# Kernel tuning notes

Hardware: AMD Instinct MI355X
Metric: run time of the kernel (lower is better)

## Reference

```python
import jax, jax.numpy as jnp
import numpy as np

B, C, H, W = 4, 384, 56, 56
K, S = 5, 7


def setup_inputs() -> dict:
    key = jax.random.key(0)
    k1, k2, k3, k4, k5 = jax.random.split(key, 5)
    x = jax.random.normal(k1, (B, C, H, W), dtype=jnp.float32)
    ctx = jax.random.normal(k2, (B, C, H, W), dtype=jnp.float32)
    # 1x1 conv weights stored as (out_ch, in_ch) matrices
    Wq = jax.random.normal(k3, (C // 2, C), dtype=jnp.float32) * (1.0 / np.sqrt(C))
    Wk = jax.random.normal(k4, (C // 2, C), dtype=jnp.float32) * (1.0 / np.sqrt(C))
    Wwd = jax.random.normal(k5, (K * K, S * S), dtype=jnp.float32) * (1.0 / np.sqrt(S * S))
    return {"x": x, "ctx": ctx, "Wq": Wq, "Wk": Wk, "Wwd": Wwd}


def reference(x, ctx, Wq, Wk, Wwd):
    b, c, h, w = x.shape
    kk = K
    # q: 1x1 conv then flatten spatial -> (B, C/2, HW)
    q = jnp.einsum('dc,bchw->bdhw', Wq, x).reshape(b, c // 2, h * w)
    # adaptive avg pool to S x S (H,W multiples of S -> uniform 8x8 bins)
    ctx_p = ctx.reshape(b, c, S, h // S, S, w // S).mean(axis=(3, 5))  # (B,C,S,S)
    kf = jnp.einsum('dc,bcst->bdst', Wk, ctx_p).reshape(b, c // 2, S * S)
    # attention over region centers: (B, HW, S*S)
    A = jax.nn.softmax(jnp.einsum('bdn,bds->bns', q, kf), axis=-1)
    # dynamic per-pixel kernels via 1x1 conv S*S -> k*k: (B, k*k, H, W)
    dyn = jnp.einsum('js,bns->bjn', Wwd, A).reshape(b, kk * kk, h, w)
    # unfold x (im2col with padding k//2) -> (B, C, k*k, H, W)
    pad = kk // 2
    xp = jnp.pad(x, ((0, 0), (0, 0), (pad, pad), (pad, pad)))
    patches = jnp.stack(
        [xp[:, :, i:i + h, j:j + w] for i in range(kk) for j in range(kk)], axis=2
    )
    # per-pixel weighted reduction over the k*k taps
    out = jnp.einsum('bcjhw,bjhw->bchw', patches, dyn)
    return out
```

## Files before the change

### kernel.cpp

```cpp
#include <hip/hip_runtime.h>

#define BB 4
#define CCH 384
#define HH 56
#define WWD 56
#define HW 3136
#define S2 49
#define S2P 52
#define D2 192
#define K2 25
#define XSP 20

__global__ __launch_bounds__(256) void gtpool_k(const float* __restrict__ Wa,
                                                const float* __restrict__ Wb,
                                                const float* __restrict__ ctx,
                                                float* __restrict__ GT,
                                                float* __restrict__ P) {
    __shared__ float As[D2 * 16];
    __shared__ float Bs[D2 * 16];
    int blk = blockIdx.x;
    int t = threadIdx.x;
    if (blk < 576) {
        int bi = blk % 24, bj = blk / 24;
        int tj = t & 15, ti = t >> 4;
#pragma unroll
        for (int k = 0; k < 3; k++) {
            int idx = t + 256 * k;
            int d = idx >> 2, q = idx & 3;
            *(float4*)&As[idx * 4] = *(const float4*)&Wa[(size_t)d * CCH + bi * 16 + 4 * q];
            *(float4*)&Bs[idx * 4] = *(const float4*)&Wb[(size_t)d * CCH + bj * 16 + 4 * q];
        }
        __syncthreads();
        float acc = 0.f;
#pragma unroll 8
        for (int d = 0; d < D2; d++)
            acc += As[d * 16 + ti] * Bs[d * 16 + tj];
        GT[(size_t)(bi * 16 + ti) * CCH + bj * 16 + tj] = acc;
    } else {
        int bs = blk - 576;
        int b = bs / S2, s = bs - b * S2;
        int sy = s / 7, sx = s % 7;
        {
            const float* p = ctx + ((size_t)(b * CCH + t)) * HW + sy * 8 * WWD + sx * 8;
            float sum = 0.f;
#pragma unroll
            for (int r = 0; r < 8; r++) {
                float4 a  = *(const float4*)(p + r * WWD);
                float4 c4 = *(const float4*)(p + r * WWD + 4);
                sum += a.x + a.y + a.z + a.w + c4.x + c4.y + c4.z + c4.w;
            }
            P[(size_t)bs * CCH + t] = sum * (1.f / 64.f);
        }
        if (t < 128) {
            int c = t + 256;
            const float* p = ctx + ((size_t)(b * CCH + c)) * HW + sy * 8 * WWD + sx * 8;
            float sum = 0.f;
#pragma unroll
            for (int r = 0; r < 8; r++) {
                float4 a  = *(const float4*)(p + r * WWD);
                float4 c4 = *(const float4*)(p + r * WWD + 4);
                sum += a.x + a.y + a.z + a.w + c4.x + c4.y + c4.z + c4.w;
            }
            P[(size_t)bs * CCH + c] = sum * (1.f / 64.f);
        }
    }
}

__global__ __launch_bounds__(256) void mv2_k(const float* __restrict__ GTt,
                                             const float* __restrict__ P,
                                             float* __restrict__ M) {
    int t = threadIdx.x;
    int r = blockIdx.x * 2 + (t >> 7);
    int c = t & 127;
    int bs0 = c, bs1 = c + 128;
    bool has1 = (bs1 < BB * S2);
    const float4* g4 = (const float4*)(GTt + (size_t)r * CCH);
    const float4* p0 = (const float4*)(P + (size_t)bs0 * CCH);
    const float4* p1 = (const float4*)(P + (size_t)(has1 ? bs1 : bs0) * CCH);
    float a0 = 0.f, a1 = 0.f, a2 = 0.f, a3 = 0.f;
#pragma unroll 8
    for (int i = 0; i < CCH / 4; i++) {
        float4 g  = g4[i];
        float4 q0 = p0[i];
        float4 q1 = p1[i];
        a0 += g.x * q0.x + g.y * q0.y;
        a1 += g.z * q0.z + g.w * q0.w;
        a2 += g.x * q1.x + g.y * q1.y;
        a3 += g.z * q1.z + g.w * q1.w;
    }
    int b0 = bs0 / S2, s0 = bs0 - b0 * S2;
    M[((size_t)(b0 * CCH + r)) * S2P + s0] = a0 + a1;
    if (has1) {
        int b1 = bs1 / S2, s1 = bs1 - b1 * S2;
        M[((size_t)(b1 * CCH + r)) * S2P + s1] = a2 + a3;
    }
    if (c >= 68 && c < 80) {
        int rem = c - 68;
        int bb = rem / 3, sp = 49 + rem % 3;
        M[((size_t)(bb * CCH + r)) * S2P + sp] = 0.f;
    }
}

__global__ __launch_bounds__(256) void attn_k(const float* __restrict__ x,
                                              const float* __restrict__ M,
                                              const float* __restrict__ Wwd,
                                              float* __restrict__ dyn) {
    __shared__ __align__(16) float smem[96 * XSP + 96 * S2P];
    __shared__ __align__(16) float sc[16 * S2P];
    __shared__ __align__(16) float wl[K2 * S2P];
    float* xs  = smem;
    float* Ms  = smem + 96 * XSP;
    float* red = smem;

    int b  = blockIdx.x / 196;
    int n0 = (blockIdx.x % 196) * 16;
    int t  = threadIdx.x;
    int pxg = t & 3, sg = (t >> 2) & 3, slice = t >> 4;

    float4 acc4[4][4];
#pragma unroll
    for (int k = 0; k < 4; k++)
#pragma unroll
        for (int j = 0; j < 4; j++) acc4[k][j] = make_float4(0.f, 0.f, 0.f, 0.f);

    const float* xb = x + (size_t)b * CCH * HW + n0;
    const float* Mb = M + (size_t)b * CCH * S2P;

#pragma unroll
    for (int k = 0; k < 5; k++) {
        int i = t + 256 * k;
        int j = i / S2P, ss = i - j * S2P;
        wl[i] = (ss < S2) ? Wwd[j * S2 + ss] : 0.f;
    }
    if (t < 20) {
        int i = t + 1280;
        int j = i / S2P, ss = i - j * S2P;
        wl[i] = (ss < S2) ? Wwd[j * S2 + ss] : 0.f;
    }

    int r0 = t >> 2, cq = t & 3;
    int r1 = (t + 256) >> 2;
    float4 px0, px1, pm0, pm1, pm2, pm3, pm4;

#define ATTN_LOAD(c0)                                                          \
    {                                                                          \
        px0 = *(const float4*)&xb[(size_t)((c0) + r0) * HW + 4 * cq];          \
        if (t < 128)                                                           \
            px1 = *(const float4*)&xb[(size_t)((c0) + r1) * HW + 4 * cq];      \
        const float* srcm = Mb + (size_t)(c0) * S2P;                           \
        pm0 = *(const float4*)&srcm[4 * t];                                    \
        pm1 = *(const float4*)&srcm[4 * (t + 256)];                            \
        pm2 = *(const float4*)&srcm[4 * (t + 512)];                            \
        pm3 = *(const float4*)&srcm[4 * (t + 768)];                            \
        if (t < 224) pm4 = *(const float4*)&srcm[4 * (t + 1024)];              \
    }

#define ATTN_WRITE()                                                           \
    {                                                                          \
        *(float4*)&xs[r0 * XSP + 4 * cq] = px0;                                \
        if (t < 128) *(float4*)&xs[r1 * XSP + 4 * cq] = px1;                   \
        *(float4*)&Ms[4 * t] = pm0;                                            \
        *(float4*)&Ms[4 * (t + 256)] = pm1;                                    \
        *(float4*)&Ms[4 * (t + 512)] = pm2;                                    \
        *(float4*)&Ms[4 * (t + 768)] = pm3;                                    \
        if (t < 224) *(float4*)&Ms[4 * (t + 1024)] = pm4;                      \
    }

    ATTN_LOAD(0);
    for (int ch = 0; ch < 4; ch++) {
        ATTN_WRITE();
        __syncthreads();
        if (ch < 3) { ATTN_LOAD((ch + 1) * 96); }
        int rbase = 6 * slice;
#pragma unroll
        for (int m = 0; m < 6; m++) {
            int r = rbase + m;
            const float4 xv = *(const float4*)&xs[r * XSP + 4 * pxg];
#pragma unroll
            for (int k = 0; k < 3; k++) {
                int g = sg + 4 * k;
                const float4 mv = *(const float4*)&Ms[r * S2P + 4 * g];
                acc4[k][0].x += mv.x * xv.x; acc4[k][0].y += mv.x * xv.y;
                acc4[k][0].z += mv.x * xv.z; acc4[k][0].w += mv.x * xv.w;
                acc4[k][1].x += mv.y * xv.x; acc4[k][1].y += mv.y * xv.y;
                acc4[k][1].z += mv.y * xv.z; acc4[k][1].w += mv.y * xv.w;
                acc4[k][2].x += mv.z * xv.x; acc4[k][2].y += mv.z * xv.y;
                acc4[k][2].z += mv.z * xv.z; acc4[k][2].w += mv.z * xv.w;
                acc4[k][3].x += mv.w * xv.x; acc4[k][3].y += mv.w * xv.y;
                acc4[k][3].z += mv.w * xv.z; acc4[k][3].w += mv.w * xv.w;
            }
            if (sg == 0) {
                const float4 mv = *(const float4*)&Ms[r * S2P + 48];
                acc4[3][0].x += mv.x * xv.x; acc4[3][0].y += mv.x * xv.y;
                acc4[3][0].z += mv.x * xv.z; acc4[3][0].w += mv.x * xv.w;
                acc4[3][1].x += mv.y * xv.x; acc4[3][1].y += mv.y * xv.y;
                acc4[3][1].z += mv.y * xv.z; acc4[3][1].w += mv.y * xv.w;
                acc4[3][2].x += mv.z * xv.x; acc4[3][2].y += mv.z * xv.y;
                acc4[3][2].z += mv.z * xv.z; acc4[3][2].w += mv.z * xv.w;
                acc4[3][3].x += mv.w * xv.x; acc4[3][3].y += mv.w * xv.y;
                acc4[3][3].z += mv.w * xv.z; acc4[3][3].w += mv.w * xv.w;
            }
        }
        __syncthreads();
    }

#pragma unroll
    for (int k = 0; k < 4; k++)
#pragma unroll
        for (int j = 0; j < 4; j++) {
            acc4[k][j].x += __shfl_xor(acc4[k][j].x, 16);
            acc4[k][j].y += __shfl_xor(acc4[k][j].y, 16);
            acc4[k][j].z += __shfl_xor(acc4[k][j].z, 16);
            acc4[k][j].w += __shfl_xor(acc4[k][j].w, 16);
            acc4[k][j].x += __shfl_xor(acc4[k][j].x, 32);
            acc4[k][j].y += __shfl_xor(acc4[k][j].y, 32);
            acc4[k][j].z += __shfl_xor(acc4[k][j].z, 32);
            acc4[k][j].w += __shfl_xor(acc4[k][j].w, 32);
        }

    if ((t & 63) < 16) {
        int wv = t >> 6;
        float* rb = red + (size_t)wv * 16 * S2P;
#pragma unroll
        for (int k = 0; k < 4; k++) {
            int g = sg + 4 * k;
            if (g < 13) {
                *(float4*)&rb[(4 * pxg + 0) * S2P + 4 * g] =
                    make_float4(acc4[k][0].x, acc4[k][1].x, acc4[k][2].x, acc4[k][3].x);
                *(float4*)&rb[(4 * pxg + 1) * S2P + 4 * g] =
                    make_float4(acc4[k][0].y, acc4[k][1].y, acc4[k][2].y, acc4[k][3].y);
                *(float4*)&rb[(4 * pxg + 2) * S2P + 4 * g] =
                    make_float4(acc4[k][0].z, acc4[k][1].z, acc4[k][2].z, acc4[k][3].z);
                *(float4*)&rb[(4 * pxg + 3) * S2P + 4 * g] =
                    make_float4(acc4[k][0].w, acc4[k][1].w, acc4[k][2].w, acc4[k][3].w);
            }
        }
    }
    __syncthreads();

    if (t < 208) {
        int px = t / 13, q = t - px * 13;
        float4 ssum = make_float4(0.f, 0.f, 0.f, 0.f);
#pragma unroll
        for (int wv = 0; wv < 4; wv++) {
            float4 vv = *(float4*)&red[(size_t)(wv * 16 + px) * S2P + 4 * q];
            ssum.x += vv.x; ssum.y += vv.y; ssum.z += vv.z; ssum.w += vv.w;
        }
        *(float4*)&sc[px * S2P + 4 * q] = ssum;
    }
    __syncthreads();

    if (t < 128) {
        int px = t >> 3, li = t & 7;
        float mx = -3.4e38f;
#pragma unroll
        for (int k = 0; k < 7; k++) { int s = li + 8 * k; if (s < S2) mx = fmaxf(mx, sc[px * S2P + s]); }
        mx = fmaxf(mx, __shfl_xor(mx, 1, 8));
        mx = fmaxf(mx, __shfl_xor(mx, 2, 8));
        mx = fmaxf(mx, __shfl_xor(mx, 4, 8));
        float e[7]; float sum = 0.f;
#pragma unroll
        for (int k = 0; k < 7; k++) {
            int s = li + 8 * k;
            if (s < S2) { e[k] = __expf(sc[px * S2P + s] - mx); sum += e[k]; }
        }
        sum += __shfl_xor(sum, 1, 8);
        sum += __shfl_xor(sum, 2, 8);
        sum += __shfl_xor(sum, 4, 8);
        float inv = 1.f / sum;
#pragma unroll
        for (int k = 0; k < 7; k++) {
            int s = li + 8 * k;
            if (s < S2) sc[px * S2P + s] = e[k] * inv;
        }
    }
    __syncthreads();

    float* dynb = dyn + (size_t)b * K2 * HW + n0;
#pragma unroll
    for (int pass = 0; pass < 2; pass++) {
        int o = t + 256 * pass;
        if (pass == 0 || t < 144) {
            int j = o >> 4, px = o & 15;
            float a = 0.f;
#pragma unroll
            for (int q = 0; q < 13; q++) {
                float4 wv = *(float4*)&wl[j * S2P + 4 * q];
                float4 pv = *(float4*)&sc[px * S2P + 4 * q];
                a += wv.x * pv.x + wv.y * pv.y + wv.z * pv.z + wv.w * pv.w;
            }
            dynb[(size_t)j * HW + px] = a;
        }
    }
#undef ATTN_LOAD
#undef ATTN_WRITE
}

__global__ __launch_bounds__(256, 3) void out_k(const float* __restrict__ x,
                                                const float* __restrict__ dyn,
                                                float* __restrict__ out) {
    __shared__ float xt[16][12][60];
    int blk    = blockIdx.x;
    int stripe = blk % 7;
    int cg     = (blk / 7) % 24;
    int b      = blk / (7 * 24);
    int h0 = stripe * 8;
    int c0 = cg * 16;
    int t  = threadIdx.x;
    const float* xb = x + ((size_t)(b * CCH + c0)) * HW;

    if (t < 192) {
        int cc = t / 12, r = t % 12;
        xt[cc][r][0] = 0.f; xt[cc][r][1] = 0.f;
        xt[cc][r][58] = 0.f; xt[cc][r][59] = 0.f;
    }
#pragma unroll
    for (int k = 0; k < 11; k++) {
        int idx = t + 256 * k;
        if (k < 10 || t < 128) {
            int cc  = idx / 168;
            int rem = idx - cc * 168;
            int r   = rem / 14;
            int q   = rem - r * 14;
            int h   = h0 - 2 + r;
            float4 v = make_float4(0.f, 0.f, 0.f, 0.f);
            if ((unsigned)h < (unsigned)HH)
                v = *(const float4*)&xb[(size_t)cc * HW + h * WWD + 4 * q];
            xt[cc][r][2 + 4 * q + 0] = v.x;
            xt[cc][r][2 + 4 * q + 1] = v.y;
            xt[cc][r][2 + 4 * q + 2] = v.z;
            xt[cc][r][2 + 4 * q + 3] = v.w;
        }
    }

    bool act = t < 224;
    int w = t % 56;
    int u = t / 56;
    int n = (h0 + 2 * u) * WWD + w;
    float dv0[K2], dv1[K2];
    if (act) {
        const float* db = dyn + (size_t)b * K2 * HW + n;
#pragma unroll
        for (int j = 0; j < K2; j++) {
            dv0[j] = db[(size_t)j * HW];
            dv1[j] = db[(size_t)j * HW + WWD];
        }
    }
    __syncthreads();
    if (!act) return;

    float* ob = out + ((size_t)(b * CCH + c0)) * HW + n;
#pragma unroll
    for (int cc = 0; cc < 16; cc++) {
        float a0 = 0.f, a1 = 0.f;
#pragma unroll
        for (int rr = 0; rr < 6; rr++) {
            int lr = 2 * u + rr;
            float v0 = xt[cc][lr][w + 0];
            float v1 = xt[cc][lr][w + 1];
            float v2 = xt[cc][lr][w + 2];
            float v3 = xt[cc][lr][w + 3];
            float v4 = xt[cc][lr][w + 4];
            if (rr < 5) {
                int o5 = rr * 5;
                a0 += v0 * dv0[o5] + v1 * dv0[o5 + 1] + v2 * dv0[o5 + 2]
                    + v3 * dv0[o5 + 3] + v4 * dv0[o5 + 4];
            }
            if (rr >= 1) {
                int o5 = (rr - 1) * 5;
                a1 += v0 * dv1[o5] + v1 * dv1[o5 + 1] + v2 * dv1[o5 + 2]
                    + v3 * dv1[o5 + 3] + v4 * dv1[o5 + 4];
            }
        }
        ob[(size_t)cc * HW] = a0;
        ob[(size_t)cc * HW + WWD] = a1;
    }
}

extern "C" void kernel_launch(void* const* d_in, const int* in_sizes, int n_in,
                              void* d_out, int out_size, void* d_ws, size_t ws_size,
                              hipStream_t stream) {
    const float* x   = (const float*)d_in[0];
    const float* ctx = (const float*)d_in[1];
    const float* Wq  = (const float*)d_in[2];
    const float* Wk  = (const float*)d_in[3];
    const float* Wwd = (const float*)d_in[4];
    float* out = (float*)d_out;
    float* ws  = (float*)d_ws;

    float* GT  = ws;
    float* M   = ws + 147456;
    float* dyn = ws + 147456 + 79872;
    float* P   = dyn;

    gtpool_k<<<576 + 196, 256, 0, stream>>>(Wq, Wk, ctx, GT, P);
    mv2_k<<<CCH / 2, 256, 0, stream>>>(GT, P, M);
    attn_k<<<BB * 196, 256, 0, stream>>>(x, M, Wwd, dyn);
    out_k<<<BB * 24 * 7, 256, 0, stream>>>(x, dyn, out);
}
```

Before: 163.3 us.

## Coalesce ctx pooling via row-strip blocks and transpose pooled layout for matvec

The pooling blocks now each cover a 32-channel group and one 8-row strip. Threads read full rows with coalesced float4 loads, store pair sums in shared memory, then reduce to the 7 pooled bins. The pooled output is written transposed (channel-major, 196 columns), so mv2_k reads it with coalesced scalar loads across threads instead of per-thread strided float4 rows. This trades the earlier scattered 8-wide reads for more blocks and a shared-memory reduction.

```diff
diff --git a/kernel.cpp b/kernel.cpp
--- a/kernel.cpp
+++ b/kernel.cpp
@@ -10,17 +10,19 @@
 #define D2 192
 #define K2 25
 #define XSP 20
+#define NBS 196
 
 __global__ __launch_bounds__(256) void gtpool_k(const float* __restrict__ Wa,
                                                 const float* __restrict__ Wb,
                                                 const float* __restrict__ ctx,
                                                 float* __restrict__ GT,
-                                                float* __restrict__ P) {
-    __shared__ float As[D2 * 16];
-    __shared__ float Bs[D2 * 16];
+                                                float* __restrict__ PT) {
+    __shared__ float sh[6144];
     int blk = blockIdx.x;
     int t = threadIdx.x;
     if (blk < 576) {
+        float* As = sh;
+        float* Bs = sh + 3072;
         int bi = blk % 24, bj = blk / 24;
         int tj = t & 15, ti = t >> 4;
 #pragma unroll
@@ -37,62 +39,59 @@
             acc += As[d * 16 + ti] * Bs[d * 16 + tj];
         GT[(size_t)(bi * 16 + ti) * CCH + bj * 16 + tj] = acc;
     } else {
-        int bs = blk - 576;
-        int b = bs / S2, s = bs - b * S2;
-        int sy = s / 7, sx = s % 7;
-        {
-            const float* p = ctx + ((size_t)(b * CCH + t)) * HW + sy * 8 * WWD + sx * 8;
+        float* part = sh;
+        int pb = blk - 576;
+        int b  = pb / 84;
+        int rem = pb - b * 84;
+        int sy = rem / 12;
+        int cg = rem - sy * 12;
+        int c0 = cg * 32;
+        const float* base = ctx + ((size_t)(b * CCH + c0)) * HW + sy * 8 * WWD;
+#pragma unroll
+        for (int k = 0; k < 14; k++) {
+            int g = t + 256 * k;
+            int cc = g / 112;
+            int r2 = g - cc * 112;
+            float4 v = *(const float4*)(base + (size_t)cc * HW + 4 * r2);
+            part[g] = (v.x + v.y) + (v.z + v.w);
+        }
+        __syncthreads();
+        if (t < 224) {
+            int cc = t / 7, sx = t - cc * 7;
             float sum = 0.f;
 #pragma unroll
             for (int r = 0; r < 8; r++) {
-                float4 a  = *(const float4*)(p + r * WWD);
-                float4 c4 = *(const float4*)(p + r * WWD + 4);
-                sum += a.x + a.y + a.z + a.w + c4.x + c4.y + c4.z + c4.w;
-            }
-            P[(size_t)bs * CCH + t] = sum * (1.f / 64.f);
-        }
-        if (t < 128) {
-            int c = t + 256;
-            const float* p = ctx + ((size_t)(b * CCH + c)) * HW + sy * 8 * WWD + sx * 8;
-            float sum = 0.f;
-#pragma unroll
-            for (int r = 0; r < 8; r++) {
-                float4 a  = *(const float4*)(p + r * WWD);
-                float4 c4 = *(const float4*)(p + r * WWD + 4);
-                sum += a.x + a.y + a.z + a.w + c4.x + c4.y + c4.z + c4.w;
-            }
-            P[(size_t)bs * CCH + c] = sum * (1.f / 64.f);
+                sum += part[cc * 112 + r * 14 + 2 * sx]
+                     + part[cc * 112 + r * 14 + 2 * sx + 1];
+            }
+            int bs = b * S2 + sy * 7 + sx;
+            PT[(size_t)(c0 + cc) * NBS + bs] = sum * (1.f / 64.f);
         }
     }
 }
 
 __global__ __launch_bounds__(256) void mv2_k(const float* __restrict__ GTt,
-                                             const float* __restrict__ P,
+                                             const float* __restrict__ PT,
                                              float* __restrict__ M) {
     int t = threadIdx.x;
     int r = blockIdx.x * 2 + (t >> 7);
     int c = t & 127;
-    int bs0 = c, bs1 = c + 128;
-    bool has1 = (bs1 < BB * S2);
-    const float4* g4 = (const float4*)(GTt + (size_t)r * CCH);
-    const float4* p0 = (const float4*)(P + (size_t)bs0 * CCH);
-    const float4* p1 = (const float4*)(P + (size_t)(has1 ? bs1 : bs0) * CCH);
-    float a0 = 0.f, a1 = 0.f, a2 = 0.f, a3 = 0.f;
+    bool has1 = (c < NBS - 128);
+    int c1 = has1 ? c + 128 : c;
+    const float* g = GTt + (size_t)r * CCH;
+    float a0 = 0.f, a1 = 0.f;
 #pragma unroll 8
-    for (int i = 0; i < CCH / 4; i++) {
-        float4 g  = g4[i];
-        float4 q0 = p0[i];
-        float4 q1 = p1[i];
-        a0 += g.x * q0.x + g.y * q0.y;
-        a1 += g.z * q0.z + g.w * q0.w;
-        a2 += g.x * q1.x + g.y * q1.y;
-        a3 += g.z * q1.z + g.w * q1.w;
-    }
-    int b0 = bs0 / S2, s0 = bs0 - b0 * S2;
-    M[((size_t)(b0 * CCH + r)) * S2P + s0] = a0 + a1;
+    for (int i = 0; i < CCH; i++) {
+        float gv = g[i];
+        a0 += gv * PT[(size_t)i * NBS + c];
+        a1 += gv * PT[(size_t)i * NBS + c1];
+    }
+    int b0 = c / S2, s0 = c - b0 * S2;
+    M[((size_t)(b0 * CCH + r)) * S2P + s0] = a0;
     if (has1) {
+        int bs1 = c + 128;
         int b1 = bs1 / S2, s1 = bs1 - b1 * S2;
-        M[((size_t)(b1 * CCH + r)) * S2P + s1] = a2 + a3;
+        M[((size_t)(b1 * CCH + r)) * S2P + s1] = a1;
     }
     if (c >= 68 && c < 80) {
         int rem = c - 68;
@@ -391,10 +390,10 @@
     float* GT  = ws;
     float* M   = ws + 147456;
     float* dyn = ws + 147456 + 79872;
-    float* P   = dyn;
-
-    gtpool_k<<<576 + 196, 256, 0, stream>>>(Wq, Wk, ctx, GT, P);
-    mv2_k<<<CCH / 2, 256, 0, stream>>>(GT, P, M);
+    float* PT  = dyn;
+
+    gtpool_k<<<576 + 336, 256, 0, stream>>>(Wq, Wk, ctx, GT, PT);
+    mv2_k<<<CCH / 2, 256, 0, stream>>>(GT, PT, M);
     attn_k<<<BB * 196, 256, 0, stream>>>(x, M, Wwd, dyn);
     out_k<<<BB * 24 * 7, 256, 0, stream>>>(x, dyn, out);
 }
```

Measured after the change: 149.4 us. 1.09x faster.
